# Kernel optimization log

Hardware: AMD Instinct MI355X
Metric: run time of the kernel (lower is better)

The kernel has to match this reference:

```python
import jax, jax.numpy as jnp
import numpy as np

N, P, E, H = 64, 1024, 512, 8
R = E // H  # head dim


def _xavier(key, shape, dtype=jnp.float32):
    fan_in, fan_out = shape[-1], shape[-2] if len(shape) > 1 else shape[-1]
    lim = jnp.sqrt(6.0 / (fan_in + fan_out)).astype(dtype)
    return jax.random.uniform(key, shape, dtype, -lim, lim)


def setup_inputs() -> dict:
    key = jax.random.key(0)
    k1, k2, k3, k4 = jax.random.split(key, 4)
    x = jax.random.normal(k1, (N, P, E), dtype=jnp.float32)
    alpha = _xavier(k2, (H, P))          # translation-invariant attention weights
    V = _xavier(k3, (H, R, E))           # per-head value projection
    W = _xavier(k4, (E, E))              # Dense kernel
    b = jnp.zeros((E,), dtype=jnp.float32)  # Dense bias
    return {"x": x, "alpha": alpha, "V": V, "W": W, "b": b}


def _log_cosh(x):
    # log(cosh(x)) = |x| + log1p(exp(-2|x|)) - log(2), numerically stable
    ax = jnp.abs(x)
    return ax + jnp.log1p(jnp.exp(-2.0 * ax)) - jnp.log(2.0).astype(x.dtype)


def reference(x, alpha, V, W, b):
    n, p, e = x.shape
    # circulant matrix: alpha_mat[h, i, j] = alpha[h, (j - i) mod P]
    # (equivalent to stacking jnp.roll(alpha, shift=i) over i)
    idx = (jnp.arange(p)[None, :] - jnp.arange(p)[:, None]) % p  # (P, P)
    alpha_mat = alpha[:, idx]                                    # (H, P, P)
    ws = jnp.einsum('hrd,npd->nhpr', V, x)                       # (N, H, P, R)
    y = jnp.einsum('hpj,nhjr->nphr', alpha_mat, ws)              # (N, P, H, R)
    y = y.reshape(n, p, -1)                                      # (N, P, E)
    y = y @ W + b
    return _log_cosh(y)
```

## Files before the change

kernel.cpp:

```cpp
#include <hip/hip_runtime.h>
#include <math.h>

typedef float f32x4 __attribute__((ext_vector_type(4)));
typedef __bf16 bf16x8 __attribute__((ext_vector_type(8)));
typedef unsigned short u16x8 __attribute__((ext_vector_type(8)));
typedef unsigned short u16x4 __attribute__((ext_vector_type(4)));

#define LN2F_ 0.69314718055994530942f

__device__ inline unsigned short f2bf(float f) {
    unsigned u = __builtin_bit_cast(unsigned, f);
    u += 0x7fffu + ((u >> 16) & 1u);
    return (unsigned short)(u >> 16);
}

__device__ inline void stage_st(unsigned short* Ls, int row, int c, u16x8 v) {
    *(u16x8*)(Ls + (row >> 4) * 512 + (((c) << 4) + ((row & 15) ^ ((c) << 1))) * 8) = v;
}
__device__ inline bf16x8 frag_ld(const unsigned short* Ls, int s, int ml, int q) {
    return __builtin_bit_cast(bf16x8,
        *(const u16x8*)(Ls + s * 512 + (((q) << 4) + (ml ^ ((q) << 1))) * 8));
}

__global__ __launch_bounds__(256) void k_cvt(const float* __restrict__ in,
                                             unsigned short* __restrict__ out, int n4) {
    int i = blockIdx.x * 256 + threadIdx.x;
    if (i >= n4) return;
    float4 v = ((const float4*)in)[i];
    u16x4 o = { f2bf(v.x), f2bf(v.y), f2bf(v.z), f2bf(v.w) };
    *(u16x4*)(out + (size_t)i * 4) = o;
}

__global__ __launch_bounds__(256) void k_build_am(const float* __restrict__ alpha,
                                                  unsigned short* __restrict__ am) {
    int t = blockIdx.x * 256 + threadIdx.x;
    int j8 = (t & 127) << 3;
    int p  = (t >> 7) & 1023;
    int h  = t >> 17;
    const float* ar = alpha + (h << 10);
    u16x8 o;
#pragma unroll
    for (int q = 0; q < 8; ++q) o[q] = f2bf(ar[(j8 + q - p) & 1023]);
    *(u16x8*)(am + ((size_t)t << 3)) = o;
}

__global__ __launch_bounds__(256) void k_build_wt(const float* __restrict__ W,
                                                  unsigned short* __restrict__ WT) {
    int t = blockIdx.x * 256 + threadIdx.x;
    int e1 = t >> 9, e = t & 511;
    WT[t] = f2bf(W[e * 512 + e1]);
}

__global__ __launch_bounds__(256) void k_gemm1(const float* __restrict__ X,
                                               const unsigned short* __restrict__ B,
                                               unsigned short* __restrict__ wsT) {
    __shared__ __align__(16) unsigned short As[128 * 32];
    __shared__ __align__(16) unsigned short Bs[128 * 32];
    const int tid = threadIdx.x;
    const int m0 = blockIdx.y * 128;
    const int e0 = blockIdx.x * 128;
    const int w = tid >> 6, lane = tid & 63, ml = lane & 15, quad = lane >> 4;
    const int wr = w >> 1, wc = w & 1;
    const int srow = tid >> 1, shalf = tid & 1;
    f32x4 acc[4][4] = {};
    for (int k0 = 0; k0 < 512; k0 += 32) {
        const float* ap = X + (size_t)(m0 + srow) * 512 + k0 + shalf * 16;
        float4 a0 = ((const float4*)ap)[0];
        float4 a1 = ((const float4*)ap)[1];
        float4 a2 = ((const float4*)ap)[2];
        float4 a3 = ((const float4*)ap)[3];
        const unsigned short* bp = B + (size_t)(e0 + srow) * 512 + k0 + shalf * 16;
        u16x8 rb0 = *(const u16x8*)bp;
        u16x8 rb1 = *(const u16x8*)(bp + 8);
        __syncthreads();
        u16x8 pa0 = { f2bf(a0.x), f2bf(a0.y), f2bf(a0.z), f2bf(a0.w),
                      f2bf(a1.x), f2bf(a1.y), f2bf(a1.z), f2bf(a1.w) };
        u16x8 pa1 = { f2bf(a2.x), f2bf(a2.y), f2bf(a2.z), f2bf(a2.w),
                      f2bf(a3.x), f2bf(a3.y), f2bf(a3.z), f2bf(a3.w) };
        stage_st(As, srow, shalf * 2 + 0, pa0);
        stage_st(As, srow, shalf * 2 + 1, pa1);
        stage_st(Bs, srow, shalf * 2 + 0, rb0);
        stage_st(Bs, srow, shalf * 2 + 1, rb1);
        __syncthreads();
        bf16x8 af[4], bfr[4];
#pragma unroll
        for (int i = 0; i < 4; ++i) {
            af[i]  = frag_ld(As, wr * 4 + i, ml, quad);
            bfr[i] = frag_ld(Bs, wc * 4 + i, ml, quad);
        }
#pragma unroll
        for (int i = 0; i < 4; ++i)
#pragma unroll
            for (int j = 0; j < 4; ++j)
                acc[i][j] = __builtin_amdgcn_mfma_f32_16x16x32_bf16(af[i], bfr[j], acc[i][j], 0, 0, 0);
    }
    const int n = m0 >> 10;
    const int pblk = m0 & 1023;
#pragma unroll
    for (int i = 0; i < 4; ++i) {
        int p = pblk + wr * 64 + i * 16 + quad * 4;
#pragma unroll
        for (int j = 0; j < 4; ++j) {
            int e = e0 + wc * 64 + j * 16 + ml;
            u16x4 o = { f2bf(acc[i][j][0]), f2bf(acc[i][j][1]),
                        f2bf(acc[i][j][2]), f2bf(acc[i][j][3]) };
            *(u16x4*)(wsT + ((size_t)n * 512 + e) * 1024 + p) = o;
        }
    }
}

__global__ __launch_bounds__(512) void k_gemm2(const unsigned short* __restrict__ wsT,
                                               const unsigned short* __restrict__ am,
                                               unsigned short* __restrict__ y) {
    __shared__ __align__(16) unsigned short As[256 * 32];
    __shared__ __align__(16) unsigned short Bs[128 * 32];
    const int tid = threadIdx.x;
    const int p0 = blockIdx.x * 128;
    const int h  = blockIdx.y;
    const int n0 = blockIdx.z * 4;
    const int w = tid >> 6, lane = tid & 63, ml = lane & 15, quad = lane >> 4;
    const int wn = w >> 1, wp = w & 1;
    const int arow = tid >> 1, ahalf = tid & 1;
    const int brow = tid >> 2, bc = tid & 3;
    const unsigned short* Ap = wsT + (size_t)(n0 + (arow >> 6)) * 524288
                                   + (size_t)(h * 64 + (arow & 63)) * 1024 + ahalf * 16;
    const unsigned short* Bp = am + ((size_t)h * 1024 + p0 + brow) * 1024 + bc * 8;
    f32x4 acc[4][4] = {};
    for (int j0 = 0; j0 < 1024; j0 += 32) {
        u16x8 ra0 = *(const u16x8*)(Ap + j0);
        u16x8 ra1 = *(const u16x8*)(Ap + j0 + 8);
        u16x8 rb  = *(const u16x8*)(Bp + j0);
        __syncthreads();
        stage_st(As, arow, ahalf * 2 + 0, ra0);
        stage_st(As, arow, ahalf * 2 + 1, ra1);
        stage_st(Bs, brow, bc, rb);
        __syncthreads();
        bf16x8 af[4], bfr[4];
#pragma unroll
        for (int mt = 0; mt < 4; ++mt)
            af[mt] = frag_ld(As, wn * 4 + mt, ml, quad);
#pragma unroll
        for (int nt = 0; nt < 4; ++nt)
            bfr[nt] = frag_ld(Bs, wp * 4 + nt, ml, quad);
#pragma unroll
        for (int mt = 0; mt < 4; ++mt)
#pragma unroll
            for (int nt = 0; nt < 4; ++nt)
                acc[mt][nt] = __builtin_amdgcn_mfma_f32_16x16x32_bf16(af[mt], bfr[nt], acc[mt][nt], 0, 0, 0);
    }
    const int n = n0 + wn;
#pragma unroll
    for (int mt = 0; mt < 4; ++mt) {
        int r0 = mt * 16 + quad * 4;
#pragma unroll
        for (int nt = 0; nt < 4; ++nt) {
            int p = p0 + wp * 64 + nt * 16 + ml;
            u16x4 o = { f2bf(acc[mt][nt][0]), f2bf(acc[mt][nt][1]),
                        f2bf(acc[mt][nt][2]), f2bf(acc[mt][nt][3]) };
            *(u16x4*)(y + ((size_t)n * 1024 + p) * 512 + h * 64 + r0) = o;
        }
    }
}

__global__ __launch_bounds__(256) void k_gemm3(const unsigned short* __restrict__ A,
                                               const unsigned short* __restrict__ B,
                                               const float* __restrict__ bias,
                                               float* __restrict__ out) {
    __shared__ __align__(16) unsigned short As[128 * 32];
    __shared__ __align__(16) unsigned short Bs[128 * 32];
    const int tid = threadIdx.x;
    const int m0 = blockIdx.y * 128;
    const int e0 = blockIdx.x * 128;
    const int w = tid >> 6, lane = tid & 63, ml = lane & 15, quad = lane >> 4;
    const int wr = w >> 1, wc = w & 1;
    const int srow = tid >> 1, shalf = tid & 1;
    f32x4 acc[4][4] = {};
    for (int k0 = 0; k0 < 512; k0 += 32) {
        const unsigned short* ap = A + (size_t)(m0 + srow) * 512 + k0 + shalf * 16;
        u16x8 ra0 = *(const u16x8*)ap;
        u16x8 ra1 = *(const u16x8*)(ap + 8);
        const unsigned short* bp = B + (size_t)(e0 + srow) * 512 + k0 + shalf * 16;
        u16x8 rb0 = *(const u16x8*)bp;
        u16x8 rb1 = *(const u16x8*)(bp + 8);
        __syncthreads();
        stage_st(As, srow, shalf * 2 + 0, ra0);
        stage_st(As, srow, shalf * 2 + 1, ra1);
        stage_st(Bs, srow, shalf * 2 + 0, rb0);
        stage_st(Bs, srow, shalf * 2 + 1, rb1);
        __syncthreads();
        bf16x8 af[4], bfr[4];
#pragma unroll
        for (int i = 0; i < 4; ++i) {
            af[i]  = frag_ld(As, wr * 4 + i, ml, quad);
            bfr[i] = frag_ld(Bs, wc * 4 + i, ml, quad);
        }
#pragma unroll
        for (int i = 0; i < 4; ++i)
#pragma unroll
            for (int j = 0; j < 4; ++j)
                acc[i][j] = __builtin_amdgcn_mfma_f32_16x16x32_bf16(af[i], bfr[j], acc[i][j], 0, 0, 0);
    }
#pragma unroll
    for (int j = 0; j < 4; ++j) {
        int e = e0 + wc * 64 + j * 16 + ml;
        float bv = bias[e];
#pragma unroll
        for (int i = 0; i < 4; ++i) {
            int mg = m0 + wr * 64 + i * 16 + quad * 4;
#pragma unroll
            for (int r = 0; r < 4; ++r) {
                float v  = acc[i][j][r] + bv;
                float ax = fabsf(v);
                float t  = __expf(-2.0f * ax);
                out[(size_t)(mg + r) * 512 + e] = ax + __logf(1.0f + t) - LN2F_;
            }
        }
    }
}

extern "C" void kernel_launch(void* const* d_in, const int* in_sizes, int n_in,
                              void* d_out, int out_size, void* d_ws, size_t ws_size,
                              hipStream_t stream) {
    const float* x     = (const float*)d_in[0];
    const float* alpha = (const float*)d_in[1];
    const float* V     = (const float*)d_in[2];
    const float* W     = (const float*)d_in[3];
    const float* b     = (const float*)d_in[4];

    unsigned short* am  = (unsigned short*)d_out;
    unsigned short* Vb  = am + 8388608;
    unsigned short* wsT = (unsigned short*)d_ws;
    unsigned short* y   = wsT + 33554432;
    unsigned short* WT  = wsT;
    float* out = (float*)d_out;

    k_cvt<<<256, 256, 0, stream>>>(V, Vb, 65536);
    k_build_am<<<4096, 256, 0, stream>>>(alpha, am);

    k_gemm1<<<dim3(4, 512), 256, 0, stream>>>(x, Vb, wsT);
    k_gemm2<<<dim3(8, 8, 16), 512, 0, stream>>>(wsT, am, y);
    k_build_wt<<<1024, 256, 0, stream>>>(W, WT);
    k_gemm3<<<dim3(4, 512), 256, 0, stream>>>(y, WT, b, out);
}
```

Measured before the change: 482.9 us.

## Retile GEMM1 and GEMM3 to 64-row by full-512-column block tiles

Both projection GEMMs change from 128x128 tiles to 64x512 tiles, so each block covers all output columns for its 64 rows and each wave owns a 64x128 slab. The activation matrix (X in fp32, y in bf16) is read and converted exactly once instead of four times, which removes redundant global reads and bf16 conversions of the large operand. In exchange each block streams the whole 512x512 weight matrix, LDS per block grows to about 36 KB, and each wave holds twice as many accumulators (128 floats), which may lower occupancy.

New measurement: 591.7 us. +22.5%, slower.

```diff
diff --git a/kernel.cpp b/kernel.cpp
--- a/kernel.cpp
+++ b/kernel.cpp
@@ -54,54 +54,54 @@
 __global__ __launch_bounds__(256) void k_gemm1(const float* __restrict__ X,
                                                const unsigned short* __restrict__ B,
                                                unsigned short* __restrict__ wsT) {
-    __shared__ __align__(16) unsigned short As[128 * 32];
-    __shared__ __align__(16) unsigned short Bs[128 * 32];
+    __shared__ __align__(16) unsigned short As[64 * 32];
+    __shared__ __align__(16) unsigned short Bs[512 * 32];
     const int tid = threadIdx.x;
-    const int m0 = blockIdx.y * 128;
-    const int e0 = blockIdx.x * 128;
+    const int m0 = blockIdx.x * 64;
     const int w = tid >> 6, lane = tid & 63, ml = lane & 15, quad = lane >> 4;
-    const int wr = w >> 1, wc = w & 1;
-    const int srow = tid >> 1, shalf = tid & 1;
-    f32x4 acc[4][4] = {};
+    const int arow = tid >> 2, ac = tid & 3;
+    const float* apb = X + (size_t)(m0 + arow) * 512 + ac * 8;
+    const unsigned short* bp0 = B + (size_t)tid * 512;
+    const unsigned short* bp1 = B + (size_t)(tid + 256) * 512;
+    f32x4 acc[4][8] = {};
     for (int k0 = 0; k0 < 512; k0 += 32) {
-        const float* ap = X + (size_t)(m0 + srow) * 512 + k0 + shalf * 16;
-        float4 a0 = ((const float4*)ap)[0];
-        float4 a1 = ((const float4*)ap)[1];
-        float4 a2 = ((const float4*)ap)[2];
-        float4 a3 = ((const float4*)ap)[3];
-        const unsigned short* bp = B + (size_t)(e0 + srow) * 512 + k0 + shalf * 16;
-        u16x8 rb0 = *(const u16x8*)bp;
-        u16x8 rb1 = *(const u16x8*)(bp + 8);
-        __syncthreads();
-        u16x8 pa0 = { f2bf(a0.x), f2bf(a0.y), f2bf(a0.z), f2bf(a0.w),
-                      f2bf(a1.x), f2bf(a1.y), f2bf(a1.z), f2bf(a1.w) };
-        u16x8 pa1 = { f2bf(a2.x), f2bf(a2.y), f2bf(a2.z), f2bf(a2.w),
-                      f2bf(a3.x), f2bf(a3.y), f2bf(a3.z), f2bf(a3.w) };
-        stage_st(As, srow, shalf * 2 + 0, pa0);
-        stage_st(As, srow, shalf * 2 + 1, pa1);
-        stage_st(Bs, srow, shalf * 2 + 0, rb0);
-        stage_st(Bs, srow, shalf * 2 + 1, rb1);
-        __syncthreads();
-        bf16x8 af[4], bfr[4];
-#pragma unroll
-        for (int i = 0; i < 4; ++i) {
-            af[i]  = frag_ld(As, wr * 4 + i, ml, quad);
-            bfr[i] = frag_ld(Bs, wc * 4 + i, ml, quad);
-        }
+        float4 a0 = ((const float4*)(apb + k0))[0];
+        float4 a1 = ((const float4*)(apb + k0))[1];
+        u16x8 rb0[4], rb1[4];
+#pragma unroll
+        for (int c = 0; c < 4; ++c) {
+            rb0[c] = *(const u16x8*)(bp0 + k0 + c * 8);
+            rb1[c] = *(const u16x8*)(bp1 + k0 + c * 8);
+        }
+        __syncthreads();
+        u16x8 pa = { f2bf(a0.x), f2bf(a0.y), f2bf(a0.z), f2bf(a0.w),
+                     f2bf(a1.x), f2bf(a1.y), f2bf(a1.z), f2bf(a1.w) };
+        stage_st(As, arow, ac, pa);
+#pragma unroll
+        for (int c = 0; c < 4; ++c) {
+            stage_st(Bs, tid, c, rb0[c]);
+            stage_st(Bs, tid + 256, c, rb1[c]);
+        }
+        __syncthreads();
+        bf16x8 af[4], bfr[8];
+#pragma unroll
+        for (int i = 0; i < 4; ++i) af[i] = frag_ld(As, i, ml, quad);
+#pragma unroll
+        for (int j = 0; j < 8; ++j) bfr[j] = frag_ld(Bs, w * 8 + j, ml, quad);
 #pragma unroll
         for (int i = 0; i < 4; ++i)
 #pragma unroll
-            for (int j = 0; j < 4; ++j)
+            for (int j = 0; j < 8; ++j)
                 acc[i][j] = __builtin_amdgcn_mfma_f32_16x16x32_bf16(af[i], bfr[j], acc[i][j], 0, 0, 0);
     }
     const int n = m0 >> 10;
     const int pblk = m0 & 1023;
 #pragma unroll
     for (int i = 0; i < 4; ++i) {
-        int p = pblk + wr * 64 + i * 16 + quad * 4;
-#pragma unroll
-        for (int j = 0; j < 4; ++j) {
-            int e = e0 + wc * 64 + j * 16 + ml;
+        int p = pblk + i * 16 + quad * 4;
+#pragma unroll
+        for (int j = 0; j < 8; ++j) {
+            int e = w * 128 + j * 16 + ml;
             u16x4 o = { f2bf(acc[i][j][0]), f2bf(acc[i][j][1]),
                         f2bf(acc[i][j][2]), f2bf(acc[i][j][3]) };
             *(u16x4*)(wsT + ((size_t)n * 512 + e) * 1024 + p) = o;
@@ -166,47 +166,50 @@
                                                const unsigned short* __restrict__ B,
                                                const float* __restrict__ bias,
                                                float* __restrict__ out) {
-    __shared__ __align__(16) unsigned short As[128 * 32];
-    __shared__ __align__(16) unsigned short Bs[128 * 32];
+    __shared__ __align__(16) unsigned short As[64 * 32];
+    __shared__ __align__(16) unsigned short Bs[512 * 32];
     const int tid = threadIdx.x;
-    const int m0 = blockIdx.y * 128;
-    const int e0 = blockIdx.x * 128;
+    const int m0 = blockIdx.x * 64;
     const int w = tid >> 6, lane = tid & 63, ml = lane & 15, quad = lane >> 4;
-    const int wr = w >> 1, wc = w & 1;
-    const int srow = tid >> 1, shalf = tid & 1;
-    f32x4 acc[4][4] = {};
+    const int arow = tid >> 2, ac = tid & 3;
+    const unsigned short* apb = A + (size_t)(m0 + arow) * 512 + ac * 8;
+    const unsigned short* bp0 = B + (size_t)tid * 512;
+    const unsigned short* bp1 = B + (size_t)(tid + 256) * 512;
+    f32x4 acc[4][8] = {};
     for (int k0 = 0; k0 < 512; k0 += 32) {
-        const unsigned short* ap = A + (size_t)(m0 + srow) * 512 + k0 + shalf * 16;
-        u16x8 ra0 = *(const u16x8*)ap;
-        u16x8 ra1 = *(const u16x8*)(ap + 8);
-        const unsigned short* bp = B + (size_t)(e0 + srow) * 512 + k0 + shalf * 16;
-        u16x8 rb0 = *(const u16x8*)bp;
-        u16x8 rb1 = *(const u16x8*)(bp + 8);
-        __syncthreads();
-        stage_st(As, srow, shalf * 2 + 0, ra0);
-        stage_st(As, srow, shalf * 2 + 1, ra1);
-        stage_st(Bs, srow, shalf * 2 + 0, rb0);
-        stage_st(Bs, srow, shalf * 2 + 1, rb1);
-        __syncthreads();
-        bf16x8 af[4], bfr[4];
+        u16x8 ra = *(const u16x8*)(apb + k0);
+        u16x8 rb0[4], rb1[4];
+#pragma unroll
+        for (int c = 0; c < 4; ++c) {
+            rb0[c] = *(const u16x8*)(bp0 + k0 + c * 8);
+            rb1[c] = *(const u16x8*)(bp1 + k0 + c * 8);
+        }
+        __syncthreads();
+        stage_st(As, arow, ac, ra);
+#pragma unroll
+        for (int c = 0; c < 4; ++c) {
+            stage_st(Bs, tid, c, rb0[c]);
+            stage_st(Bs, tid + 256, c, rb1[c]);
+        }
+        __syncthreads();
+        bf16x8 af[4], bfr[8];
+#pragma unroll
+        for (int i = 0; i < 4; ++i) af[i] = frag_ld(As, i, ml, quad);
+#pragma unroll
+        for (int j = 0; j < 8; ++j) bfr[j] = frag_ld(Bs, w * 8 + j, ml, quad);
+#pragma unroll
+        for (int i = 0; i < 4; ++i)
+#pragma unroll
+            for (int j = 0; j < 8; ++j)
+                acc[i][j] = __builtin_amdgcn_mfma_f32_16x16x32_bf16(af[i], bfr[j], acc[i][j], 0, 0, 0);
+    }
+#pragma unroll
+    for (int j = 0; j < 8; ++j) {
+        int e = w * 128 + j * 16 + ml;
+        float bv = bias[e];
 #pragma unroll
         for (int i = 0; i < 4; ++i) {
-            af[i]  = frag_ld(As, wr * 4 + i, ml, quad);
-            bfr[i] = frag_ld(Bs, wc * 4 + i, ml, quad);
-        }
-#pragma unroll
-        for (int i = 0; i < 4; ++i)
-#pragma unroll
-            for (int j = 0; j < 4; ++j)
-                acc[i][j] = __builtin_amdgcn_mfma_f32_16x16x32_bf16(af[i], bfr[j], acc[i][j], 0, 0, 0);
-    }
-#pragma unroll
-    for (int j = 0; j < 4; ++j) {
-        int e = e0 + wc * 64 + j * 16 + ml;
-        float bv = bias[e];
-#pragma unroll
-        for (int i = 0; i < 4; ++i) {
-            int mg = m0 + wr * 64 + i * 16 + quad * 4;
+            int mg = m0 + i * 16 + quad * 4;
 #pragma unroll
             for (int r = 0; r < 4; ++r) {
                 float v  = acc[i][j][r] + bv;
@@ -237,8 +240,8 @@
     k_cvt<<<256, 256, 0, stream>>>(V, Vb, 65536);
     k_build_am<<<4096, 256, 0, stream>>>(alpha, am);
 
-    k_gemm1<<<dim3(4, 512), 256, 0, stream>>>(x, Vb, wsT);
+    k_gemm1<<<dim3(1024), 256, 0, stream>>>(x, Vb, wsT);
     k_gemm2<<<dim3(8, 8, 16), 512, 0, stream>>>(wsT, am, y);
     k_build_wt<<<1024, 256, 0, stream>>>(W, WT);
-    k_gemm3<<<dim3(4, 512), 256, 0, stream>>>(y, WT, b, out);
-}
+    k_gemm3<<<dim3(1024), 256, 0, stream>>>(y, WT, b, out);
+}
```
